# Kernel optimization log

Measured on AMD Instinct MI355X. Metric: run time of the kernel, lower is better.

Reference implementation:

```python
import jax, jax.numpy as jnp
import numpy as np

N, C, H, W = 8, 256, 64, 64
EPS = 1e-5


def setup_inputs() -> dict:
    key = jax.random.key(0)
    ks = jax.random.split(key, 11)
    s = 0.02
    return {
        "x": jax.random.normal(ks[0], (N, C, H, W), dtype=jnp.float32),
        "ln_w": jnp.ones((C, H, W), dtype=jnp.float32),
        "ln_b": jnp.zeros((C, H, W), dtype=jnp.float32),
        "wq": jax.random.normal(ks[1], (C, C), dtype=jnp.float32) * s,
        "bq": jnp.zeros((C,), dtype=jnp.float32),
        "wk": jax.random.normal(ks[2], (C, C), dtype=jnp.float32) * s,
        "bk": jnp.zeros((C,), dtype=jnp.float32),
        "wv": jax.random.normal(ks[3], (C, C), dtype=jnp.float32) * s,
        "bv": jnp.zeros((C,), dtype=jnp.float32),
        "wo": jax.random.normal(ks[4], (C, C), dtype=jnp.float32) * s,
        "bo": jnp.zeros((C,), dtype=jnp.float32),
    }


def _conv1x1(x, w, b):
    # x: [n,c,h,w], w: [out,in], b: [out]  (1x1 conv == per-pixel matmul)
    return jnp.einsum("nchw,oc->nohw", x, w) + b[None, :, None, None]


def reference(x, ln_w, ln_b, wq, bq, wk, bk, wv, bv, wo, bo):
    n, c, h, w = x.shape
    # LayerNorm over (C,H,W)
    mu = jnp.mean(x, axis=(1, 2, 3), keepdims=True)
    var = jnp.var(x, axis=(1, 2, 3), keepdims=True)
    nx = (x - mu) * jax.lax.rsqrt(var + EPS) * ln_w[None] + ln_b[None]

    q = _conv1x1(nx, wq, bq).reshape(n, c, h * w)  # [n,c,hw]
    k = _conv1x1(nx, wk, bk).reshape(n, c, h * w)
    v = _conv1x1(nx, wv, bv).reshape(n, c, h * w)

    scale = 1.0 / jnp.sqrt(jnp.float32(c))
    qk = jnp.einsum("nci,ncj->nij", q, k) * scale       # [n,hw,hw]
    attn = jax.nn.softmax(qk, axis=-1)
    res = jnp.einsum("nij,ncj->nci", attn, v)           # [n,c,hw]
    res = res.reshape(n, c, h, w)
    res = _conv1x1(res, wo, bo)
    return x + res
```

## Files before the change

kernel.cpp:

```cpp
#include <hip/hip_runtime.h>
#include <hip/hip_bf16.h>

#define N_ 8
#define C_ 256
#define HW_ 4096
#define CNT_ (C_*HW_)

typedef __attribute__((ext_vector_type(8))) short bf16x8;
typedef __attribute__((ext_vector_type(4))) float f32x4;
typedef __attribute__((ext_vector_type(16))) float f32x16;
typedef __attribute__((ext_vector_type(4))) int i32x4;
typedef __attribute__((ext_vector_type(8))) int i32x8;

__device__ inline float exp2fast(float x){ return __builtin_amdgcn_exp2f(x); }

__device__ inline unsigned short f2bf(float f){
  union{float f; unsigned u;} v; v.f=f;
  unsigned r = v.u + 0x7fff + ((v.u>>16)&1);
  return (unsigned short)(r>>16);
}
__device__ inline float bf2f(unsigned short h){
  union{unsigned u; float f;} v; v.u = ((unsigned)h)<<16; return v.f;
}

__device__ inline f32x4 mfma16(bf16x8 a, bf16x8 b, f32x4 c){
  return __builtin_amdgcn_mfma_f32_16x16x32_bf16(a,b,c,0,0,0);
}
__device__ inline f32x16 mfma_mx(i32x8 a, i32x8 b, f32x16 c){
  return __builtin_amdgcn_mfma_scale_f32_32x32x64_f8f6f4(a, b, c, 0, 0, 0, 127, 0, 127);
}

__device__ inline i32x8 ld2x4(const char* p){
  i32x4 a = *(const i32x4*)p;
  i32x4 b = *(const i32x4*)(p+16);
  i32x8 r;
  r[0]=a[0]; r[1]=a[1]; r[2]=a[2]; r[3]=a[3];
  r[4]=b[0]; r[5]=b[1]; r[6]=b[2]; r[7]=b[3];
  return r;
}

#define GLL16(gp, lp) __builtin_amdgcn_global_load_lds( \
    (__attribute__((address_space(1))) void*)(gp), \
    (__attribute__((address_space(3))) void*)(lp), 16, 0, 0)

__global__ void k_cvt(const float* __restrict__ src, unsigned short* __restrict__ dst){
  int i = blockIdx.x*256 + threadIdx.x;
  dst[i] = f2bf(src[i]);
}

__global__ void k_stats1(const float* __restrict__ x, float2* __restrict__ part){
  int n = blockIdx.x >> 8;
  int chunk = blockIdx.x & 255;
  const float4* p = (const float4*)(x + (size_t)n*CNT_ + (size_t)chunk*4096);
  int t = threadIdx.x;
  float s=0.f, s2=0.f;
  #pragma unroll
  for(int i=0;i<4;i++){
    float4 v = p[t + 256*i];
    s  += v.x+v.y+v.z+v.w;
    s2 += v.x*v.x+v.y*v.y+v.z*v.z+v.w*v.w;
  }
  #pragma unroll
  for(int o=32;o;o>>=1){ s += __shfl_down(s,o); s2 += __shfl_down(s2,o); }
  __shared__ float sh[4], sh2[4];
  int lane = t&63, wid = t>>6;
  if(lane==0){ sh[wid]=s; sh2[wid]=s2; }
  __syncthreads();
  if(t==0){
    float2 r; r.x = sh[0]+sh[1]+sh[2]+sh[3]; r.y = sh2[0]+sh2[1]+sh2[2]+sh2[3];
    part[blockIdx.x] = r;
  }
}

__global__ void k_stats2(const float2* __restrict__ part, float2* __restrict__ stats){
  int n = blockIdx.x, t = threadIdx.x;
  float2 v = part[n*256 + t];
  float s = v.x, s2 = v.y;
  #pragma unroll
  for(int o=32;o;o>>=1){ s += __shfl_down(s,o); s2 += __shfl_down(s2,o); }
  __shared__ float sh[4], sh2[4];
  int lane = t&63, wid = t>>6;
  if(lane==0){ sh[wid]=s; sh2[wid]=s2; }
  __syncthreads();
  if(t==0){
    s = sh[0]+sh[1]+sh[2]+sh[3];
    s2 = sh2[0]+sh2[1]+sh2[2]+sh2[3];
    float mean = s * (1.f/(float)CNT_);
    float var  = s2 * (1.f/(float)CNT_) - mean*mean;
    float2 r; r.x = mean; r.y = rsqrtf(var + 1e-5f);
    stats[n] = r;
  }
}

__global__ void k_norm(const float* __restrict__ x, const float* __restrict__ lnw,
                       const float* __restrict__ lnb, const float2* __restrict__ stats,
                       unsigned short* __restrict__ nx){
  __shared__ float tile[64][65];
  int n = blockIdx.z, c0 = blockIdx.y*64, p0 = blockIdx.x*64;
  float2 st = stats[n];
  float mu = st.x, rs = st.y;
  int t = threadIdx.x, col = t&63, rw = t>>6;
  #pragma unroll
  for(int pass=0; pass<16; pass++){
    int row = pass*4 + rw;
    size_t gi = (size_t)(c0+row)*HW_ + (p0+col);
    float v = x[(size_t)n*CNT_ + gi];
    tile[row][col] = (v - mu)*rs*lnw[gi] + lnb[gi];
  }
  __syncthreads();
  #pragma unroll
  for(int pass=0; pass<16; pass++){
    int prow = pass*4 + rw;
    nx[((size_t)n*HW_ + p0+prow)*C_ + c0 + col] = f2bf(tile[col][prow]);
  }
}

__device__ inline void g2_stage(const char* A, const char* B, char* buf,
                                int w, int r8, int s8, int i0, int c0, int kb0){
  int sl = (s8 ^ (r8&7)) << 4;
  #pragma unroll
  for(int q=0;q<4;q++){
    int row = w*32 + q*8 + r8;
    GLL16(A + (size_t)(i0+row)*512 + kb0 + sl, buf + w*4096 + q*1024);
    GLL16(B + (size_t)(c0+row)*512 + kb0 + sl, buf + 16384 + w*4096 + q*1024);
  }
}

template<int BIAS_ROW, int OUT_MODE>
__global__ __launch_bounds__(256, 2) void k_gemm2(
    const unsigned short* __restrict__ Ab, long sA,
    const unsigned short* __restrict__ Bb, long sB,
    const float* __restrict__ bias, float scale,
    void* __restrict__ Outb, long sO, int ldo,
    float* __restrict__ foutb, const float* __restrict__ xres){
  __shared__ __align__(16) char lds[65536];
  int n = blockIdx.z;
  const char* A = (const char*)(Ab + (size_t)n*sA);
  const char* B = (const char*)(Bb + (size_t)n*sB);
  int t = threadIdx.x, w = t>>6, l = t&63;
  int wr = w>>1, wc = w&1, ri = l&15, kq = l>>4;
  int r8 = l>>3, s8 = l&7;
  int i0 = blockIdx.x*128, c0 = blockIdx.y*128;

  f32x4 acc[4][4];
  #pragma unroll
  for(int m=0;m<4;m++)
    #pragma unroll
    for(int nn=0;nn<4;nn++)
      #pragma unroll
      for(int r=0;r<4;r++) acc[m][nn][r] = 0.f;

  g2_stage(A, B, lds, w, r8, s8, i0, c0, 0);
  __syncthreads();

  for(int kt=0; kt<4; ++kt){
    char* buf = lds + (kt&1)*32768;
    if (kt < 3) g2_stage(A, B, lds + ((kt&1)^1)*32768, w, r8, s8, i0, c0, (kt+1)*128);
    __builtin_amdgcn_s_setprio(1);
    #pragma unroll
    for(int kc=0;kc<2;kc++){
      bf16x8 af[4], bfv[4];
      #pragma unroll
      for(int m=0;m<4;m++){
        int row = wr*64 + m*16 + ri;
        af[m] = *(const bf16x8*)(buf + row*128 + ((((kc<<2)|kq) ^ (row&7))<<4));
      }
      #pragma unroll
      for(int nn=0;nn<4;nn++){
        int row = wc*64 + nn*16 + ri;
        bfv[nn] = *(const bf16x8*)(buf + 16384 + row*128 + ((((kc<<2)|kq) ^ (row&7))<<4));
      }
      #pragma unroll
      for(int m=0;m<4;m++)
        #pragma unroll
        for(int nn=0;nn<4;nn++)
          acc[m][nn] = mfma16(af[m], bfv[nn], acc[m][nn]);
    }
    __builtin_amdgcn_s_setprio(0);
    __syncthreads();
  }

  if (OUT_MODE == 2){
    float* fout = foutb + (size_t)n*sO;
    const float* xr = xres + (size_t)n*sO;
    #pragma unroll
    for(int m=0;m<4;m++){
      #pragma unroll
      for(int nn=0;nn<4;nn++){
        #pragma unroll
        for(int r=0;r<4;r++){
          int row = i0 + wr*64 + m*16 + kq*4 + r;
          int col = c0 + wc*64 + nn*16 + ri;
          size_t idx = (size_t)row*ldo + col;
          fout[idx] = acc[m][nn][r] + bias[row] + xr[idx];
        }
      }
    }
  } else if (OUT_MODE == 1){
    unsigned char* O8 = (unsigned char*)Outb + (size_t)n*sO;
    #pragma unroll
    for(int m=0;m<4;m++){
      #pragma unroll
      for(int nn=0;nn<4;nn++){
        #pragma unroll
        for(int r=0;r<4;r++){
          int row = i0 + wr*64 + m*16 + kq*4 + r;
          int col = c0 + wc*64 + nn*16 + ri;
          float d = (acc[m][nn][r] + bias[BIAS_ROW ? row : col])*scale;
          unsigned u;
          asm("v_cvt_pk_fp8_f32 %0, %1, %2" : "=v"(u) : "v"(d), "v"(0.f));
          O8[(size_t)row*ldo + col] = (unsigned char)(u & 0xff);
        }
      }
    }
  } else {
    unsigned short* O = (unsigned short*)Outb + (size_t)n*sO;
    #pragma unroll
    for(int m=0;m<4;m++){
      #pragma unroll
      for(int nn=0;nn<4;nn++){
        #pragma unroll
        for(int r=0;r<4;r++){
          int row = i0 + wr*64 + m*16 + kq*4 + r;
          int col = c0 + wc*64 + nn*16 + ri;
          float d = (acc[m][nn][r] + bias[BIAS_ROW ? row : col])*scale;
          O[(size_t)row*ldo + col] = f2bf(d);
        }
      }
    }
  }
}

__device__ inline void stage_KV_mx(const char* kb, const char* vb, char* buf,
                                   int w, int l, int j0){
  #pragma unroll
  for(int k=0;k<4;k++){
    int g = w*4 + k;
    int row = g*4 + (l>>4);
    int i = l & 15;
    int sp = (((i>>1) ^ (row&7))<<5) + ((i&1)<<4);
    GLL16(kb + (size_t)(j0+row)*256 + sp, buf + g*1024);
  }
  #pragma unroll
  for(int k=0;k<5;k++){
    int g = w*5 + k;
    int c = g*64 + l;
    int d = c/5; int sg = c - d*5; sg = (sg==4)?0:sg;
    GLL16(vb + (size_t)d*HW_ + j0 + sg*16, buf + 16384 + g*1024);
  }
}

__global__ __launch_bounds__(256, 2) void k_attn8(const unsigned char* __restrict__ qt,
                                                  const unsigned char* __restrict__ kt,
                                                  const unsigned char* __restrict__ vv,
                                                  unsigned short* __restrict__ pO0,
                                                  unsigned short* __restrict__ pO1,
                                                  float2* __restrict__ pml){
  __shared__ __align__(16) char lds[73728];
  int t = threadIdx.x, w = t>>6, l = t&63, hi = l>>5, lo5 = l&31;
  int nb = blockIdx.x & 7, rem = blockIdx.x >> 3;
  int qb = rem >> 1, jh = rem & 1;
  int q0 = qb*128 + w*32;
  const char* kb = (const char*)(kt + (size_t)nb*HW_*C_);
  const char* vb = (const char*)(vv + (size_t)nb*(size_t)CNT_);
  const char* qp = (const char*)(qt + (size_t)nb*HW_*C_);
  int jbase = jh*2048;

  i32x8 qfr[4];
  #pragma unroll
  for(int db=0; db<4; db++)
    qfr[db] = ld2x4(qp + (size_t)(q0+lo5)*256 + db*64 + hi*32);

  f32x16 o[8];
  #pragma unroll
  for(int dt=0;dt<8;dt++){
    #pragma unroll
    for(int r=0;r<16;r++) o[dt][r]=0.f;
  }
  float m = -1e30f, lsum = 0.f;

  stage_KV_mx(kb, vb, lds, w, l, jbase);
  __syncthreads();

  for(int it=0; it<32; ++it){
    char* bufc = lds + (it&1)*36864;
    if (it < 31) stage_KV_mx(kb, vb, lds + ((it&1)^1)*36864, w, l, jbase + (it+1)*64);

    f32x16 Sa, Sb;
    #pragma unroll
    for(int r=0;r<16;r++){ Sa[r]=0.f; Sb[r]=0.f; }
    __builtin_amdgcn_s_setprio(1);
    #pragma unroll
    for(int db=0; db<4; db++){
      int sl = ((db*2+hi) ^ (lo5&7))<<5;
      i32x8 ka  = ld2x4(bufc + lo5*256      + sl);
      i32x8 kb2 = ld2x4(bufc + (32+lo5)*256 + sl);
      Sa = mfma_mx(ka,  qfr[db], Sa);
      Sb = mfma_mx(kb2, qfr[db], Sb);
    }
    __builtin_amdgcn_s_setprio(0);

    float mm[8];
    #pragma unroll
    for(int r=0;r<8;r++) mm[r] = fmaxf(fmaxf(Sa[r],Sa[r+8]), fmaxf(Sb[r],Sb[r+8]));
    mm[0]=fmaxf(mm[0],mm[4]); mm[1]=fmaxf(mm[1],mm[5]);
    mm[2]=fmaxf(mm[2],mm[6]); mm[3]=fmaxf(mm[3],mm[7]);
    float mx = fmaxf(fmaxf(mm[0],mm[1]), fmaxf(mm[2],mm[3]));
    { float mA = mx, mB = mx;
      asm("v_permlane32_swap_b32 %0, %1" : "+v"(mA), "+v"(mB));
      mx = fmaxf(mA, mB); }
    if (!__all(mx <= m + 8.f)){
      float mn = fmaxf(m, mx);
      float al = exp2fast(m - mn);
      lsum *= al;
      #pragma unroll
      for(int dt=0;dt<8;dt++) o[dt] = o[dt] * al;
      m = mn;
    }
    float rs = 0.f;
    #pragma unroll
    for(int r=0;r<16;r++){
      Sa[r] = exp2fast(Sa[r]-m); rs += Sa[r];
      Sb[r] = exp2fast(Sb[r]-m); rs += Sb[r];
    }
    { float rA = rs, rB = rs;
      asm("v_permlane32_swap_b32 %0, %1" : "+v"(rA), "+v"(rB));
      lsum += rA + rB; }

    unsigned Aw[4], Bw[4];
    #pragma unroll
    for(int w4=0; w4<4; w4++){
      unsigned ua, ub;
      asm("v_cvt_pk_fp8_f32 %0, %1, %2" : "=v"(ua) : "v"(Sa[4*w4]), "v"(Sa[4*w4+1]));
      asm("v_cvt_pk_fp8_f32 %0, %1, %2 op_sel:[0,0,1]" : "+v"(ua) : "v"(Sa[4*w4+2]), "v"(Sa[4*w4+3]));
      asm("v_cvt_pk_fp8_f32 %0, %1, %2" : "=v"(ub) : "v"(Sb[4*w4]), "v"(Sb[4*w4+1]));
      asm("v_cvt_pk_fp8_f32 %0, %1, %2 op_sel:[0,0,1]" : "+v"(ub) : "v"(Sb[4*w4+2]), "v"(Sb[4*w4+3]));
      Aw[w4] = ua; Bw[w4] = ub;
    }
    #pragma unroll
    for(int w4=0; w4<4; w4++)
      asm("v_permlane32_swap_b32 %0, %1" : "+v"(Aw[w4]), "+v"(Bw[w4]));
    i32x8 P;
    P[0]=Aw[0]; P[1]=Bw[0]; P[2]=Aw[1]; P[3]=Bw[1];
    P[4]=Aw[2]; P[5]=Bw[2]; P[6]=Aw[3]; P[7]=Bw[3];

    __builtin_amdgcn_s_setprio(1);
    #pragma unroll
    for(int dt=0;dt<8;dt++){
      i32x8 vf = ld2x4(bufc + 16384 + (dt*32+lo5)*80 + hi*32);
      o[dt] = mfma_mx(vf, P, o[dt]);
    }
    __builtin_amdgcn_s_setprio(0);
    __syncthreads();
  }

  unsigned short* pb = (jh ? pO1 : pO0) + ((size_t)nb*HW_ + q0 + lo5)*C_;
  #pragma unroll
  for(int dt=0;dt<8;dt++){
    #pragma unroll
    for(int g=0;g<4;g++){
      int d0 = dt*32 + g*8 + hi*4;
      unsigned short h0 = f2bf(o[dt][4*g]);
      unsigned short h1 = f2bf(o[dt][4*g+1]);
      unsigned short h2 = f2bf(o[dt][4*g+2]);
      unsigned short h3 = f2bf(o[dt][4*g+3]);
      uint2 uo; uo.x = (unsigned)h0 | ((unsigned)h1<<16);
      uo.y = (unsigned)h2 | ((unsigned)h3<<16);
      *(uint2*)(pb + d0) = uo;
    }
  }
  if (l < 32){
    float2 ml; ml.x = m; ml.y = lsum;
    pml[(size_t)jh*32768 + (size_t)nb*HW_ + q0 + lo5] = ml;
  }
}

__global__ void k_merge(unsigned short* __restrict__ pO0,
                        const unsigned short* __restrict__ pO1,
                        const float2* __restrict__ pml){
  int t = threadIdx.x;
  int row = blockIdx.x*8 + (t>>5);
  int dn = t & 31;
  float2 ml0 = pml[row], ml1 = pml[32768 + row];
  float mN = fmaxf(ml0.x, ml1.x);
  float a0 = exp2fast(ml0.x - mN), a1 = exp2fast(ml1.x - mN);
  float inv = 1.f/(a0*ml0.y + a1*ml1.y);
  float s0 = a0*inv, s1 = a1*inv;
  size_t off = (size_t)row*256 + dn*8;
  uint4 u0 = *(const uint4*)(pO0 + off);
  uint4 u1 = *(const uint4*)(pO1 + off);
  unsigned r[4];
  unsigned w0[4] = {u0.x, u0.y, u0.z, u0.w};
  unsigned w1[4] = {u1.x, u1.y, u1.z, u1.w};
  #pragma unroll
  for(int q=0;q<4;q++){
    float lo = s0*bf2f((unsigned short)(w0[q]&0xffff)) + s1*bf2f((unsigned short)(w1[q]&0xffff));
    float hi = s0*bf2f((unsigned short)(w0[q]>>16))    + s1*bf2f((unsigned short)(w1[q]>>16));
    r[q] = (unsigned)f2bf(lo) | ((unsigned)f2bf(hi)<<16);
  }
  uint4 ru; ru.x=r[0]; ru.y=r[1]; ru.z=r[2]; ru.w=r[3];
  *(uint4*)(pO0 + off) = ru;
}

extern "C" void kernel_launch(void* const* d_in, const int* in_sizes, int n_in,
                              void* d_out, int out_size, void* d_ws, size_t ws_size,
                              hipStream_t stream) {
  const float* x   = (const float*)d_in[0];
  const float* lnw = (const float*)d_in[1];
  const float* lnb = (const float*)d_in[2];
  const float* wq  = (const float*)d_in[3];
  const float* bq  = (const float*)d_in[4];
  const float* wk  = (const float*)d_in[5];
  const float* bk  = (const float*)d_in[6];
  const float* wv  = (const float*)d_in[7];
  const float* bv  = (const float*)d_in[8];
  const float* wo  = (const float*)d_in[9];
  const float* bo  = (const float*)d_in[10];
  float* out = (float*)d_out;

  uintptr_t base = (uintptr_t)d_ws;
  float2* part  = (float2*)base;
  float2* stats = (float2*)(base + 16384);
  unsigned short* wqb = (unsigned short*)(base + 16448);
  unsigned short* wkb = wqb + 65536;
  unsigned short* wvb = wqb + 2*65536;
  unsigned short* wob = wqb + 3*65536;
  unsigned short* nx  = wqb + 4*65536;
  const size_t TEN = (size_t)N_*HW_*C_;
  unsigned short* qtb = nx + TEN;
  unsigned short* ktb = qtb + TEN;
  unsigned short* vvb = ktb + TEN;
  unsigned short* pO1 = vvb + TEN;
  float2* pml = (float2*)(pO1 + TEN);
  unsigned short* rest = nx;

  k_cvt<<<dim3(256),256,0,stream>>>(wq, wqb);
  k_cvt<<<dim3(256),256,0,stream>>>(wk, wkb);
  k_cvt<<<dim3(256),256,0,stream>>>(wv, wvb);
  k_cvt<<<dim3(256),256,0,stream>>>(wo, wob);

  k_stats1<<<dim3(2048),256,0,stream>>>(x, part);
  k_stats2<<<dim3(8),256,0,stream>>>(part, stats);
  k_norm<<<dim3(64,4,8),256,0,stream>>>(x, lnw, lnb, stats, nx);

  k_gemm2<0,1><<<dim3(32,2,8),256,0,stream>>>(nx, (long)(HW_*C_), wqb, 0L, bq, 0.3002807f,
                                              qtb, (long)(HW_*C_), C_, nullptr, nullptr);
  k_gemm2<0,1><<<dim3(32,2,8),256,0,stream>>>(nx, (long)(HW_*C_), wkb, 0L, bk, 0.3002807f,
                                              ktb, (long)(HW_*C_), C_, nullptr, nullptr);
  k_gemm2<1,1><<<dim3(2,32,8),256,0,stream>>>(wvb, 0L, nx, (long)(HW_*C_), bv, 1.0f,
                                              vvb, (long)(CNT_), HW_, nullptr, nullptr);

  k_attn8<<<dim3(512),256,0,stream>>>((const unsigned char*)qtb, (const unsigned char*)ktb,
                                      (const unsigned char*)vvb, rest, pO1, pml);
  k_merge<<<dim3(4096),256,0,stream>>>(rest, pO1, pml);

  k_gemm2<1,2><<<dim3(2,32,8),256,0,stream>>>(wob, 0L, rest, (long)(HW_*C_), bo, 1.0f,
                                              nullptr, (long)(CNT_), HW_, out, x);
}
```

Before: 173.3 us.

## Fuse split-attention merge into output projection and consolidate small prep kernels

The separate merge pass that combined the two partial attention outputs is removed. The output-projection GEMM now reads both bf16 partials and their max/sum statistics, rescales and combines them in registers while staging B tiles into LDS, then does the residual add. This avoids writing and re-reading the merged tensor. The four weight-conversion launches become one, and the stats-finalize kernel is folded into the norm kernel, where every block redundantly reduces the 256 partials. The trade-off is doubled B-operand global traffic in the GEMM, plus register-path loads in place of async LDS loads for B.

```diff
diff --git a/kernel.cpp b/kernel.cpp
--- a/kernel.cpp
+++ b/kernel.cpp
@@ -43,9 +43,12 @@
     (__attribute__((address_space(1))) void*)(gp), \
     (__attribute__((address_space(3))) void*)(lp), 16, 0, 0)
 
-__global__ void k_cvt(const float* __restrict__ src, unsigned short* __restrict__ dst){
+__global__ void k_cvtall(const float* __restrict__ s0, const float* __restrict__ s1,
+                         const float* __restrict__ s2, const float* __restrict__ s3,
+                         unsigned short* __restrict__ dst){
   int i = blockIdx.x*256 + threadIdx.x;
-  dst[i] = f2bf(src[i]);
+  const float* s = (i < 65536) ? s0 : (i < 131072) ? s1 : (i < 196608) ? s2 : s3;
+  dst[i] = f2bf(s[i & 65535]);
 }
 
 __global__ void k_stats1(const float* __restrict__ x, float2* __restrict__ part){
@@ -72,34 +75,33 @@
   }
 }
 
-__global__ void k_stats2(const float2* __restrict__ part, float2* __restrict__ stats){
-  int n = blockIdx.x, t = threadIdx.x;
-  float2 v = part[n*256 + t];
-  float s = v.x, s2 = v.y;
-  #pragma unroll
-  for(int o=32;o;o>>=1){ s += __shfl_down(s,o); s2 += __shfl_down(s2,o); }
-  __shared__ float sh[4], sh2[4];
-  int lane = t&63, wid = t>>6;
-  if(lane==0){ sh[wid]=s; sh2[wid]=s2; }
-  __syncthreads();
-  if(t==0){
-    s = sh[0]+sh[1]+sh[2]+sh[3];
-    s2 = sh2[0]+sh2[1]+sh2[2]+sh2[3];
-    float mean = s * (1.f/(float)CNT_);
-    float var  = s2 * (1.f/(float)CNT_) - mean*mean;
-    float2 r; r.x = mean; r.y = rsqrtf(var + 1e-5f);
-    stats[n] = r;
-  }
-}
-
 __global__ void k_norm(const float* __restrict__ x, const float* __restrict__ lnw,
-                       const float* __restrict__ lnb, const float2* __restrict__ stats,
+                       const float* __restrict__ lnb, const float2* __restrict__ part,
                        unsigned short* __restrict__ nx){
   __shared__ float tile[64][65];
+  __shared__ float2 stsh;
   int n = blockIdx.z, c0 = blockIdx.y*64, p0 = blockIdx.x*64;
-  float2 st = stats[n];
-  float mu = st.x, rs = st.y;
   int t = threadIdx.x, col = t&63, rw = t>>6;
+  {
+    float2 v = part[n*256 + t];
+    float s = v.x, s2 = v.y;
+    #pragma unroll
+    for(int o=32;o;o>>=1){ s += __shfl_down(s,o); s2 += __shfl_down(s2,o); }
+    __shared__ float sh[4], sh2[4];
+    int lane = t&63, wid = t>>6;
+    if(lane==0){ sh[wid]=s; sh2[wid]=s2; }
+    __syncthreads();
+    if(t==0){
+      s = sh[0]+sh[1]+sh[2]+sh[3];
+      s2 = sh2[0]+sh2[1]+sh2[2]+sh2[3];
+      float mean = s * (1.f/(float)CNT_);
+      float var  = s2 * (1.f/(float)CNT_) - mean*mean;
+      float2 r; r.x = mean; r.y = rsqrtf(var + 1e-5f);
+      stsh = r;
+    }
+    __syncthreads();
+  }
+  float mu = stsh.x, rs = stsh.y;
   #pragma unroll
   for(int pass=0; pass<16; pass++){
     int row = pass*4 + rw;
@@ -131,8 +133,7 @@
     const unsigned short* __restrict__ Ab, long sA,
     const unsigned short* __restrict__ Bb, long sB,
     const float* __restrict__ bias, float scale,
-    void* __restrict__ Outb, long sO, int ldo,
-    float* __restrict__ foutb, const float* __restrict__ xres){
+    void* __restrict__ Outb, long sO, int ldo){
   __shared__ __align__(16) char lds[65536];
   int n = blockIdx.z;
   const char* A = (const char*)(Ab + (size_t)n*sA);
@@ -180,23 +181,7 @@
     __syncthreads();
   }
 
-  if (OUT_MODE == 2){
-    float* fout = foutb + (size_t)n*sO;
-    const float* xr = xres + (size_t)n*sO;
-    #pragma unroll
-    for(int m=0;m<4;m++){
-      #pragma unroll
-      for(int nn=0;nn<4;nn++){
-        #pragma unroll
-        for(int r=0;r<4;r++){
-          int row = i0 + wr*64 + m*16 + kq*4 + r;
-          int col = c0 + wc*64 + nn*16 + ri;
-          size_t idx = (size_t)row*ldo + col;
-          fout[idx] = acc[m][nn][r] + bias[row] + xr[idx];
-        }
-      }
-    }
-  } else if (OUT_MODE == 1){
+  if (OUT_MODE == 1){
     unsigned char* O8 = (unsigned char*)Outb + (size_t)n*sO;
     #pragma unroll
     for(int m=0;m<4;m++){
@@ -226,6 +211,138 @@
           float d = (acc[m][nn][r] + bias[BIAS_ROW ? row : col])*scale;
           O[(size_t)row*ldo + col] = f2bf(d);
         }
+      }
+    }
+  }
+}
+
+__global__ __launch_bounds__(256, 2) void k_outproj2(
+    const unsigned short* __restrict__ wob,
+    const unsigned short* __restrict__ pO0, const unsigned short* __restrict__ pO1,
+    const float2* __restrict__ pml,
+    const float* __restrict__ bo, const float* __restrict__ x,
+    float* __restrict__ out){
+  __shared__ __align__(16) char lds[65536];
+  int n = blockIdx.z;
+  const char* A = (const char*)wob;
+  const char* B0 = (const char*)(pO0 + (size_t)n*HW_*C_);
+  const char* B1 = (const char*)(pO1 + (size_t)n*HW_*C_);
+  int t = threadIdx.x, w = t>>6, l = t&63;
+  int wr = w>>1, wc = w&1, ri = l&15, kq = l>>4;
+  int r8 = l>>3, s8 = l&7;
+  int i0 = blockIdx.x*128, c0 = blockIdx.y*128;
+  int sl = (s8 ^ (r8&7)) << 4;
+
+  float s0v[4], s1v[4];
+  #pragma unroll
+  for(int q=0;q<4;q++){
+    int row = c0 + w*32 + q*8 + r8;
+    float2 ml0 = pml[(size_t)n*HW_ + row];
+    float2 ml1 = pml[(size_t)N_*HW_ + (size_t)n*HW_ + row];
+    float mN = fmaxf(ml0.x, ml1.x);
+    float a0 = exp2fast(ml0.x - mN), a1 = exp2fast(ml1.x - mN);
+    float inv = 1.f/(a0*ml0.y + a1*ml1.y);
+    s0v[q] = a0*inv; s1v[q] = a1*inv;
+  }
+
+  f32x4 acc[4][4];
+  #pragma unroll
+  for(int m=0;m<4;m++)
+    #pragma unroll
+    for(int nn=0;nn<4;nn++)
+      #pragma unroll
+      for(int r=0;r<4;r++) acc[m][nn][r] = 0.f;
+
+  uint4 bl0[4], bl1[4];
+  #pragma unroll
+  for(int q=0;q<4;q++){
+    int row = w*32 + q*8 + r8;
+    GLL16(A + (size_t)(i0+row)*512 + sl, lds + w*4096 + q*1024);
+    bl0[q] = *(const uint4*)(B0 + (size_t)(c0+row)*512 + sl);
+    bl1[q] = *(const uint4*)(B1 + (size_t)(c0+row)*512 + sl);
+  }
+  #pragma unroll
+  for(int q=0;q<4;q++){
+    unsigned w0[4] = {bl0[q].x, bl0[q].y, bl0[q].z, bl0[q].w};
+    unsigned w1[4] = {bl1[q].x, bl1[q].y, bl1[q].z, bl1[q].w};
+    uint4 rw;
+    unsigned rr[4];
+    #pragma unroll
+    for(int j=0;j<4;j++){
+      float lo = s0v[q]*bf2f((unsigned short)(w0[j]&0xffff)) + s1v[q]*bf2f((unsigned short)(w1[j]&0xffff));
+      float hi = s0v[q]*bf2f((unsigned short)(w0[j]>>16))    + s1v[q]*bf2f((unsigned short)(w1[j]>>16));
+      rr[j] = (unsigned)f2bf(lo) | ((unsigned)f2bf(hi)<<16);
+    }
+    rw.x=rr[0]; rw.y=rr[1]; rw.z=rr[2]; rw.w=rr[3];
+    *(uint4*)(lds + 16384 + w*4096 + q*1024 + l*16) = rw;
+  }
+  __syncthreads();
+
+  for(int kt=0; kt<4; ++kt){
+    char* buf  = lds + (kt&1)*32768;
+    char* nbuf = lds + ((kt&1)^1)*32768;
+    if (kt < 3){
+      int kb0 = (kt+1)*128;
+      #pragma unroll
+      for(int q=0;q<4;q++){
+        int row = w*32 + q*8 + r8;
+        GLL16(A + (size_t)(i0+row)*512 + kb0 + sl, nbuf + w*4096 + q*1024);
+        bl0[q] = *(const uint4*)(B0 + (size_t)(c0+row)*512 + kb0 + sl);
+        bl1[q] = *(const uint4*)(B1 + (size_t)(c0+row)*512 + kb0 + sl);
+      }
+    }
+    __builtin_amdgcn_s_setprio(1);
+    #pragma unroll
+    for(int kc=0;kc<2;kc++){
+      bf16x8 af[4], bfv[4];
+      #pragma unroll
+      for(int m=0;m<4;m++){
+        int row = wr*64 + m*16 + ri;
+        af[m] = *(const bf16x8*)(buf + row*128 + ((((kc<<2)|kq) ^ (row&7))<<4));
+      }
+      #pragma unroll
+      for(int nn=0;nn<4;nn++){
+        int row = wc*64 + nn*16 + ri;
+        bfv[nn] = *(const bf16x8*)(buf + 16384 + row*128 + ((((kc<<2)|kq) ^ (row&7))<<4));
+      }
+      #pragma unroll
+      for(int m=0;m<4;m++)
+        #pragma unroll
+        for(int nn=0;nn<4;nn++)
+          acc[m][nn] = mfma16(af[m], bfv[nn], acc[m][nn]);
+    }
+    __builtin_amdgcn_s_setprio(0);
+    if (kt < 3){
+      #pragma unroll
+      for(int q=0;q<4;q++){
+        unsigned w0[4] = {bl0[q].x, bl0[q].y, bl0[q].z, bl0[q].w};
+        unsigned w1[4] = {bl1[q].x, bl1[q].y, bl1[q].z, bl1[q].w};
+        unsigned rr[4];
+        #pragma unroll
+        for(int j=0;j<4;j++){
+          float lo = s0v[q]*bf2f((unsigned short)(w0[j]&0xffff)) + s1v[q]*bf2f((unsigned short)(w1[j]&0xffff));
+          float hi = s0v[q]*bf2f((unsigned short)(w0[j]>>16))    + s1v[q]*bf2f((unsigned short)(w1[j]>>16));
+          rr[j] = (unsigned)f2bf(lo) | ((unsigned)f2bf(hi)<<16);
+        }
+        uint4 rw; rw.x=rr[0]; rw.y=rr[1]; rw.z=rr[2]; rw.w=rr[3];
+        *(uint4*)(nbuf + 16384 + w*4096 + q*1024 + l*16) = rw;
+      }
+    }
+    __syncthreads();
+  }
+
+  const float* xr = x + (size_t)n*CNT_;
+  float* fout = out + (size_t)n*CNT_;
+  #pragma unroll
+  for(int m=0;m<4;m++){
+    #pragma unroll
+    for(int nn=0;nn<4;nn++){
+      #pragma unroll
+      for(int r=0;r<4;r++){
+        int row = i0 + wr*64 + m*16 + kq*4 + r;
+        int col = c0 + wc*64 + nn*16 + ri;
+        size_t idx = (size_t)row*HW_ + col;
+        fout[idx] = acc[m][nn][r] + bo[row] + xr[idx];
       }
     }
   }
@@ -371,35 +488,8 @@
   }
   if (l < 32){
     float2 ml; ml.x = m; ml.y = lsum;
-    pml[(size_t)jh*32768 + (size_t)nb*HW_ + q0 + lo5] = ml;
-  }
-}
-
-__global__ void k_merge(unsigned short* __restrict__ pO0,
-                        const unsigned short* __restrict__ pO1,
-                        const float2* __restrict__ pml){
-  int t = threadIdx.x;
-  int row = blockIdx.x*8 + (t>>5);
-  int dn = t & 31;
-  float2 ml0 = pml[row], ml1 = pml[32768 + row];
-  float mN = fmaxf(ml0.x, ml1.x);
-  float a0 = exp2fast(ml0.x - mN), a1 = exp2fast(ml1.x - mN);
-  float inv = 1.f/(a0*ml0.y + a1*ml1.y);
-  float s0 = a0*inv, s1 = a1*inv;
-  size_t off = (size_t)row*256 + dn*8;
-  uint4 u0 = *(const uint4*)(pO0 + off);
-  uint4 u1 = *(const uint4*)(pO1 + off);
-  unsigned r[4];
-  unsigned w0[4] = {u0.x, u0.y, u0.z, u0.w};
-  unsigned w1[4] = {u1.x, u1.y, u1.z, u1.w};
-  #pragma unroll
-  for(int q=0;q<4;q++){
-    float lo = s0*bf2f((unsigned short)(w0[q]&0xffff)) + s1*bf2f((unsigned short)(w1[q]&0xffff));
-    float hi = s0*bf2f((unsigned short)(w0[q]>>16))    + s1*bf2f((unsigned short)(w1[q]>>16));
-    r[q] = (unsigned)f2bf(lo) | ((unsigned)f2bf(hi)<<16);
-  }
-  uint4 ru; ru.x=r[0]; ru.y=r[1]; ru.z=r[2]; ru.w=r[3];
-  *(uint4*)(pO0 + off) = ru;
+    pml[(size_t)jh*((size_t)N_*HW_) + (size_t)nb*HW_ + q0 + lo5] = ml;
+  }
 }
 
 extern "C" void kernel_launch(void* const* d_in, const int* in_sizes, int n_in,
@@ -420,7 +510,6 @@
 
   uintptr_t base = (uintptr_t)d_ws;
   float2* part  = (float2*)base;
-  float2* stats = (float2*)(base + 16384);
   unsigned short* wqb = (unsigned short*)(base + 16448);
   unsigned short* wkb = wqb + 65536;
   unsigned short* wvb = wqb + 2*65536;
@@ -432,28 +521,22 @@
   unsigned short* vvb = ktb + TEN;
   unsigned short* pO1 = vvb + TEN;
   float2* pml = (float2*)(pO1 + TEN);
-  unsigned short* rest = nx;
-
-  k_cvt<<<dim3(256),256,0,stream>>>(wq, wqb);
-  k_cvt<<<dim3(256),256,0,stream>>>(wk, wkb);
-  k_cvt<<<dim3(256),256,0,stream>>>(wv, wvb);
-  k_cvt<<<dim3(256),256,0,stream>>>(wo, wob);
+  unsigned short* pO0 = nx;
+
+  k_cvtall<<<dim3(1024),256,0,stream>>>(wq, wk, wv, wo, wqb);
 
   k_stats1<<<dim3(2048),256,0,stream>>>(x, part);
-  k_stats2<<<dim3(8),256,0,stream>>>(part, stats);
-  k_norm<<<dim3(64,4,8),256,0,stream>>>(x, lnw, lnb, stats, nx);
+  k_norm<<<dim3(64,4,8),256,0,stream>>>(x, lnw, lnb, part, nx);
 
   k_gemm2<0,1><<<dim3(32,2,8),256,0,stream>>>(nx, (long)(HW_*C_), wqb, 0L, bq, 0.3002807f,
-                                              qtb, (long)(HW_*C_), C_, nullptr, nullptr);
+                                              qtb, (long)(HW_*C_), C_);
   k_gemm2<0,1><<<dim3(32,2,8),256,0,stream>>>(nx, (long)(HW_*C_), wkb, 0L, bk, 0.3002807f,
-                                              ktb, (long)(HW_*C_), C_, nullptr, nullptr);
+                                              ktb, (long)(HW_*C_), C_);
   k_gemm2<1,1><<<dim3(2,32,8),256,0,stream>>>(wvb, 0L, nx, (long)(HW_*C_), bv, 1.0f,
-                                              vvb, (long)(CNT_), HW_, nullptr, nullptr);
+                                              vvb, (long)(CNT_), HW_);
 
   k_attn8<<<dim3(512),256,0,stream>>>((const unsigned char*)qtb, (const unsigned char*)ktb,
-                                      (const unsigned char*)vvb, rest, pO1, pml);
-  k_merge<<<dim3(4096),256,0,stream>>>(rest, pO1, pml);
-
-  k_gemm2<1,2><<<dim3(2,32,8),256,0,stream>>>(wob, 0L, rest, (long)(HW_*C_), bo, 1.0f,
-                                              nullptr, (long)(CNT_), HW_, out, x);
-}
+                                      (const unsigned char*)vvb, pO0, pO1, pml);
+
+  k_outproj2<<<dim3(2,32,8),256,0,stream>>>(wob, pO0, pO1, pml, bo, x, out);
+}
```

New measurement: 163.8 us. 5.5% less time.
